# Optimization experiments

Hardware: AMD Instinct MI355X
Metric: run time of the kernel (lower is better)

Reference implementation:

```python
import jax, jax.numpy as jnp
import numpy as np
from jax import lax

D_MODEL=1024; D_STATE=128; D_CONV=4; EXPAND=2; HEADDIM=64
D_INNER=EXPAND*D_MODEL; NHEADS=D_INNER//HEADDIM
POOL=64; SUMDIM=256; TAU1=0.5; TAU2=0.4

def rmsnorm(x, w, eps):
    return x * lax.rsqrt(jnp.mean(x*x, axis=-1, keepdims=True) + eps) * w

def silu(x):
    return x * jax.nn.sigmoid(x)

def setup_inputs():
    key = jax.random.key(0)
    ks = jax.random.split(key, 20)
    B, T = 4, 2048
    d_in_proj = 2*D_INNER + 2*D_STATE + NHEADS
    inp = {
        'x': jax.random.normal(ks[0], (B, T, D_MODEL), jnp.float32),
        'pool': jnp.zeros((B, POOL, SUMDIM), jnp.float32),
        'priorities': jnp.zeros((B, POOL), jnp.float32),
        'counts': jnp.zeros((B,), jnp.int32),
        'norm_w': jnp.ones((D_MODEL,), jnp.float32),
        'in_w': jax.random.normal(ks[1], (d_in_proj, D_MODEL), jnp.float32)*0.02,
        'conv_w': jax.random.normal(ks[2], (D_INNER+2*D_STATE, 1, D_CONV), jnp.float32)*0.1,
        'conv_b': jnp.zeros((D_INNER+2*D_STATE,), jnp.float32),
        'dt_bias': jax.random.uniform(ks[3], (NHEADS,), jnp.float32, -5.0, -1.0),
        'A_log': jnp.log(jax.random.uniform(ks[4], (NHEADS,), jnp.float32, 1.0, 16.0)),
        'Dp': jax.random.normal(ks[5], (NHEADS,), jnp.float32)*0.1 + 1.0,
        'ssm_norm_w': jnp.ones((D_INNER,), jnp.float32),
        'out_w': jax.random.normal(ks[6], (D_MODEL, D_INNER), jnp.float32)*0.02,
        'score_w1': jax.random.normal(ks[7], (D_MODEL//4, D_MODEL), jnp.float32)*0.03,
        'score_w2': jax.random.normal(ks[8], (1, D_MODEL//4), jnp.float32)*0.06,
        'summ_w': jax.random.normal(ks[9], (SUMDIM, D_MODEL), jnp.float32)*0.03,
        'q_w': jax.random.normal(ks[10], (SUMDIM, D_MODEL), jnp.float32)*0.03,
        'k_w': jax.random.normal(ks[11], (SUMDIM, SUMDIM), jnp.float32)*0.06,
        'v_w': jax.random.normal(ks[12], (D_MODEL, SUMDIM), jnp.float32)*0.06,
        'gate_w': jax.random.normal(ks[13], (D_MODEL, 2*D_MODEL), jnp.float32)*0.02,
    }
    return inp

def mamba2(u, in_w, conv_w, conv_b, dt_bias, A_log, Dp, ssm_norm_w, out_w):
    B, T, _ = u.shape
    zxbcdt = u @ in_w.T                      # [B,T,2*d_inner+2*d_state+nheads]
    z = zxbcdt[..., :D_INNER]
    xBC = zxbcdt[..., D_INNER:2*D_INNER+2*D_STATE]
    dt = jax.nn.softplus(zxbcdt[..., 2*D_INNER+2*D_STATE:] + dt_bias)  # [B,T,H]
    # causal depthwise conv over time
    xc = jnp.transpose(xBC, (0, 2, 1))       # [B,C,T]
    xc = lax.conv_general_dilated(xc, conv_w, (1,), [(D_CONV-1, 0)],
                                  dimension_numbers=('NCH', 'OIH', 'NCH'),
                                  feature_group_count=D_INNER+2*D_STATE)
    xBC = silu(jnp.transpose(xc + conv_b[None, :, None], (0, 2, 1)))
    xh = xBC[..., :D_INNER].reshape(B, T, NHEADS, HEADDIM)
    Bm = xBC[..., D_INNER:D_INNER+D_STATE]   # [B,T,N]
    Cm = xBC[..., D_INNER+D_STATE:]          # [B,T,N]
    A = -jnp.exp(A_log)                      # [H]
    dA = jnp.exp(dt * A)                     # [B,T,H]
    def step(h, inp):
        dA_t, dt_t, x_t, B_t, C_t = inp      # [B,H],[B,H],[B,H,P],[B,N],[B,N]
        h = dA_t[:, :, None, None]*h + (dt_t[:, :, None]*x_t)[..., None]*B_t[:, None, None, :]
        y = jnp.einsum('bhpn,bn->bhp', h, C_t)
        return h, y
    h0 = jnp.zeros((B, NHEADS, HEADDIM, D_STATE), u.dtype)
    xs = (jnp.swapaxes(dA, 0, 1), jnp.swapaxes(dt, 0, 1), jnp.swapaxes(xh, 0, 1),
          jnp.swapaxes(Bm, 0, 1), jnp.swapaxes(Cm, 0, 1))
    _, ys = lax.scan(step, h0, xs)           # [T,B,H,P]
    y = jnp.swapaxes(ys, 0, 1) + Dp[None, None, :, None]*xh
    y = y.reshape(B, T, D_INNER)
    y = rmsnorm(y * silu(z), ssm_norm_w, 1e-5)
    return y @ out_w.T

def pool_update(tokens, scores, pool, priorities, counts,
                summ_w):
    B, T, D = tokens.shape
    mask = scores > TAU1
    order = jnp.argsort(-scores, axis=1)     # descending
    s_scores = jnp.take_along_axis(scores, order, 1)
    s_tokens = jnp.take_along_axis(tokens, order[..., None], 1)
    s_mask = jnp.take_along_axis(mask, order, 1)
    summaries = s_tokens @ summ_w.T          # [B,T,SUMDIM]
    nslots = min(T, POOL)
    bidx = jnp.arange(B)
    def slot_step(carry, inp):
        pool, pri, counts = carry
        has_imp, imp, summ = inp             # [B],[B],[B,SUMDIM]
        add = has_imp & (counts < POOL)
        widx = jnp.minimum(counts, POOL-1)
        pool = pool.at[bidx, widx].set(jnp.where(add[:, None], summ, pool[bidx, widx]))
        pri = pri.at[bidx, widx].set(jnp.where(add, imp, pri[bidx, widx]))
        counts = counts + add.astype(counts.dtype)
        replace = has_imp & (counts >= POOL)
        min_idx = jnp.argmin(pri, axis=1)
        min_p = pri[bidx, min_idx]
        should = replace & (imp > min_p)
        pool = pool.at[bidx, min_idx].set(jnp.where(should[:, None], summ, pool[bidx, min_idx]))
        pri = pri.at[bidx, min_idx].set(jnp.where(should, imp, pri[bidx, min_idx]))
        return (pool, pri, counts), None
    xs = (jnp.swapaxes(s_mask[:, :nslots], 0, 1),
          jnp.swapaxes(s_scores[:, :nslots], 0, 1),
          jnp.swapaxes(summaries[:, :nslots], 0, 1))
    (pool, priorities, counts), _ = lax.scan(slot_step, (pool, priorities, counts), xs)
    return pool, priorities, counts

def reference(x, pool, priorities, counts, norm_w, in_w, conv_w, conv_b, dt_bias,
              A_log, Dp, ssm_norm_w, out_w, score_w1, score_w2, summ_w,
              q_w, k_w, v_w, gate_w):
    B = x.shape[0]
    y = x + mamba2(rmsnorm(x, norm_w, 1e-4), in_w, conv_w, conv_b, dt_bias,
                   A_log, Dp, ssm_norm_w, out_w)
    scores = jax.nn.sigmoid(jnp.maximum(y @ score_w1.T, 0.0) @ score_w2.T)[..., 0]
    # layer_idx % cross_layer_frequency == 0 -> update path taken
    pool, priorities, counts = pool_update(y, scores, pool, priorities, counts, summ_w)
    mask = jnp.arange(POOL)[None, :] < counts[:, None]
    q = y @ q_w.T                            # [B,T,S]
    k = pool @ k_w.T                         # [B,P,S]
    v = pool @ v_w.T                         # [B,P,D]
    attn = jnp.einsum('bts,bps->btp', q, k) / (SUMDIM ** 0.5)
    attn = jnp.where(mask[:, None, :], attn, -jnp.inf)
    attn = jnp.nan_to_num(jax.nn.softmax(attn, axis=-1), nan=0.0)
    retrieved = jnp.einsum('btp,bpd->btd', attn, v)
    gate = jax.nn.sigmoid(jnp.concatenate([y, retrieved], axis=-1) @ gate_w.T)
    rmask = ((jnp.mean(scores, axis=1) > TAU2) & (counts > 0)).astype(y.dtype)[:, None, None]
    y = y + gate * retrieved * rmask
    return (y, pool, priorities, counts)
```

## Files before the change

kernel.cpp:

```cpp
#include <hip/hip_runtime.h>


using u16 = unsigned short;
using f16x8 = __attribute__((ext_vector_type(8))) _Float16;
using f32x4  = __attribute__((ext_vector_type(4))) float;

#define DEV __device__ __forceinline__

#define GLOAD4(g, l)  __builtin_amdgcn_global_load_lds((const __attribute__((address_space(1))) void*)(g), (__attribute__((address_space(3))) void*)(l), 4, 0, 0)
#define GLOAD16(g, l) __builtin_amdgcn_global_load_lds((const __attribute__((address_space(1))) void*)(g), (__attribute__((address_space(3))) void*)(l), 16, 0, 0)
#define VMWAIT(N) asm volatile("s_waitcnt vmcnt(" #N ")" ::: "memory")

static constexpr int Bb = 4, T = 2048, D = 1024;
static constexpr int DIN = 2048, DST = 128, NH = 32;
static constexpr int DPROJ = 4384;
static constexpr int CCH = 2304;
static constexpr int ROWS = Bb * T;
static constexpr int NC = 8, CL = 256;
static constexpr float RSC = 4096.f, RSCI = 1.f / 4096.f;

DEV u16 f2h_bits(float f) { union { _Float16 h; u16 u; } v; v.h = (_Float16)f; return v.u; }
DEV float h2f(u16 u) { union { _Float16 h; u16 u; } v; v.u = u; return (float)v.h; }
DEV double sigd(double x) { return 1.0 / (1.0 + exp(-x)); }
DEV float sigf(float x) { return 1.f / (1.f + expf(-x)); }
DEV int swz(int c) { return c ^ ((c >> 3) & 3); }

__global__ void diag_kernel(float* o, float v) { if (threadIdx.x == 0) o[0] = v; }
__global__ void zerod_kernel(double* p, int n) { if ((int)threadIdx.x < n) p[threadIdx.x] = 0.0; }

__global__ void split2_kernel(const float* __restrict__ in, u16* __restrict__ out, long n) {
    long i = (long)blockIdx.x * 256 + threadIdx.x;
    if (i >= n) return;
    float v = in[i];
    u16 h = f2h_bits(v);
    float r1 = (v - h2f(h)) * RSC;
    out[i] = h;
    out[n + i] = f2h_bits(r1);
}

__global__ __launch_bounds__(256) void rms_x_kernel(const float* __restrict__ x, const float* __restrict__ w,
                                                    u16* __restrict__ up, long pstride) {
    long row = blockIdx.x; int tid = threadIdx.x;
    const float* xr = x + row * D;
    float4 xv = *(const float4*)(xr + tid * 4);
    double ss = (double)xv.x * xv.x + (double)xv.y * xv.y + (double)xv.z * xv.z + (double)xv.w * xv.w;
    for (int off = 1; off < 64; off <<= 1) ss += __shfl_xor(ss, off);
    __shared__ double tmp[4];
    if ((tid & 63) == 0) tmp[tid >> 6] = ss;
    __syncthreads();
    double tot = tmp[0] + tmp[1] + tmp[2] + tmp[3];
    double scale = 1.0 / sqrt(tot / (double)D + 1e-4);
    float4 wv = *(const float4*)(w + tid * 4);
    long base = row * D + tid * 4;
    float vals[4];
    vals[0] = (float)((double)xv.x * scale * (double)wv.x);
    vals[1] = (float)((double)xv.y * scale * (double)wv.y);
    vals[2] = (float)((double)xv.z * scale * (double)wv.z);
    vals[3] = (float)((double)xv.w * scale * (double)wv.w);
#pragma unroll
    for (int j = 0; j < 4; j++) {
        float f = vals[j];
        u16 h = f2h_bits(f);
        up[base + j] = h;
        up[pstride + base + j] = f2h_bits((f - h2f(h)) * RSC);
    }
}

template <int NP>
DEV void stage_one(u16* s0, u16* s1, const float* __restrict__ src, long ld,
                   int row0, int lastrow, int k0, int tid) {
    int r = tid >> 1, cb = (tid & 1) * 2;
    long rg = row0 + r; if (rg > lastrow) rg = lastrow;
    const float* p = src + rg * ld + k0 + cb * 8;
    u16 h16[16], l16[16];
#pragma unroll
    for (int q = 0; q < 4; q++) {
        float4 v4 = *(const float4*)(p + q * 4);
        float vv[4] = { v4.x, v4.y, v4.z, v4.w };
#pragma unroll
        for (int j = 0; j < 4; j++) {
            float xv = vv[j];
            u16 h = f2h_bits(xv);
            h16[q * 4 + j] = h;
            if constexpr (NP == 2) l16[q * 4 + j] = f2h_bits((xv - h2f(h)) * RSC);
        }
    }
    int o0 = swz(r * 4 + cb) * 8, o1 = swz(r * 4 + cb + 1) * 8;
    *(uint4*)(s0 + o0) = *(const uint4*)(h16);
    *(uint4*)(s0 + o1) = *(const uint4*)(h16 + 8);
    if constexpr (NP == 2) {
        *(uint4*)(s1 + o0) = *(const uint4*)(l16);
        *(uint4*)(s1 + o1) = *(const uint4*)(l16 + 8);
    }
}

DEV void stage_pre_dma(u16* dst, const u16* __restrict__ src, long ld,
                       int row0, int lastrow, int k0, int wid, int lane) {
#pragma unroll
    for (int j = 0; j < 2; j++) {
        int s = wid * 128 + j * 64 + lane;
        int g = swz(s);
        int r = g >> 2, cs = g & 3;
        long rg = row0 + r; if (rg > lastrow) rg = lastrow;
        const u16* gp = src + rg * ld + k0 + cs * 8;
        GLOAD16(gp, dst + (wid * 128 + j * 64) * 8);
    }
}

#define STAGE_TILE(bb, k0_) do { \
    u16* As0_ = (bb); \
    u16* As1_ = (bb) + 4096; \
    u16* Bs0_ = (bb) + NP * 4096; \
    u16* Bs1_ = (bb) + NP * 4096 + 4096; \
    if constexpr (BP) { \
        stage_pre_dma(Bs0_, Bp, K, tN, N - 1, (k0_), wid, lane); \
        if constexpr (NP == 2) stage_pre_dma(Bs1_, Bp + bstride, K, tN, N - 1, (k0_), wid, lane); \
    } \
    if constexpr (AP) { \
        stage_pre_dma(As0_, Ap, K, tM, M - 1, (k0_), wid, lane); \
        if constexpr (NP == 2) stage_pre_dma(As1_, Ap + astride, K, tM, M - 1, (k0_), wid, lane); \
    } else { \
        stage_one<NP>(As0_, NP == 2 ? As1_ : nullptr, A, lda, tM, M - 1, (k0_), tid); \
    } \
    if constexpr (!BP) { \
        stage_one<NP>(Bs0_, NP == 2 ? Bs1_ : nullptr, B, ldb, tN, N - 1, (k0_), tid); \
    } \
} while (0)

template <int NP, int MODE, bool BP, bool AP>
__global__ __launch_bounds__(256, 2) void gemm_f32(
    const float* __restrict__ A, long lda,
    const u16* __restrict__ Ap, size_t astride,
    const float* __restrict__ B, long ldb,
    const u16* __restrict__ Bp, size_t bstride,
    int M, int N, int K,
    float* __restrict__ out0, float* __restrict__ out1,
    const float* __restrict__ aux0, const float* __restrict__ aux1,
    float* __restrict__ dtb, float* __restrict__ dab) {
    __shared__ __align__(16) u16 sm[2 * NP * 2 * 4096];
    int tid = threadIdx.x, lane = tid & 63, wid = tid >> 6;
    int wr = wid >> 1, wc = wid & 1;
    int nwg = gridDim.x * gridDim.y;
    int wg = blockIdx.y * gridDim.x + blockIdx.x;
    int lin = (wg & 7) * (nwg >> 3) + (wg >> 3);
    int tM = (lin / gridDim.x) * 128, tN = (lin % gridDim.x) * 128;

    f32x4 acc1[4][4], acc2[4][4];
#pragma unroll
    for (int i = 0; i < 4; i++)
#pragma unroll
        for (int j = 0; j < 4; j++) {
            acc1[i][j] = f32x4{0.f, 0.f, 0.f, 0.f};
            if constexpr (NP == 2) acc2[i][j] = f32x4{0.f, 0.f, 0.f, 0.f};
        }

    int rA = wr * 64 + (lane & 15);
    int rB = wc * 64 + (lane & 15);
    int kc = lane >> 4;
    int oA[4], oB[4];
#pragma unroll
    for (int i = 0; i < 4; i++) {
        oA[i] = swz((rA + i * 16) * 4 + kc) * 8;
        oB[i] = swz((rB + i * 16) * 4 + kc) * 8;
    }

    int nsteps = K / 32;
    int cur = 0;
    STAGE_TILE(sm, 0);
    __syncthreads();
    for (int kt = 0; kt < nsteps; ++kt) {
        u16* cb = sm + cur * (NP * 2 * 4096);
        if (kt + 1 < nsteps) {
            u16* nb = sm + (cur ^ 1) * (NP * 2 * 4096);
            STAGE_TILE(nb, (kt + 1) * 32);
        }
        u16* As0 = cb; u16* As1 = cb + 4096;
        u16* Bs0 = cb + NP * 4096; u16* Bs1 = cb + NP * 4096 + 4096;
        f16x8 fa[4], fb[4];
#pragma unroll
        for (int i = 0; i < 4; i++) {
            fa[i] = *(const f16x8*)(As0 + oA[i]);
            fb[i] = *(const f16x8*)(Bs0 + oB[i]);
        }
#pragma unroll
        for (int mi = 0; mi < 4; mi++)
#pragma unroll
            for (int ni = 0; ni < 4; ni++)
                acc1[mi][ni] = __builtin_amdgcn_mfma_f32_16x16x32_f16(fa[mi], fb[ni], acc1[mi][ni], 0, 0, 0);
        if constexpr (NP == 2) {
#pragma unroll
            for (int i = 0; i < 4; i++) fb[i] = *(const f16x8*)(Bs1 + oB[i]);
#pragma unroll
            for (int mi = 0; mi < 4; mi++)
#pragma unroll
                for (int ni = 0; ni < 4; ni++)
                    acc2[mi][ni] = __builtin_amdgcn_mfma_f32_16x16x32_f16(fa[mi], fb[ni], acc2[mi][ni], 0, 0, 0);
#pragma unroll
            for (int i = 0; i < 4; i++) {
                fa[i] = *(const f16x8*)(As1 + oA[i]);
                fb[i] = *(const f16x8*)(Bs0 + oB[i]);
            }
#pragma unroll
            for (int mi = 0; mi < 4; mi++)
#pragma unroll
                for (int ni = 0; ni < 4; ni++)
                    acc2[mi][ni] = __builtin_amdgcn_mfma_f32_16x16x32_f16(fa[mi], fb[ni], acc2[mi][ni], 0, 0, 0);
        }
        if (kt + 1 < nsteps) {
            __syncthreads();
            cur ^= 1;
        }
    }
    int laneh = lane >> 4, lanel = lane & 15;
#pragma unroll
    for (int mi = 0; mi < 4; mi++)
#pragma unroll
        for (int ni = 0; ni < 4; ni++) {
            int col = tN + wc * 64 + ni * 16 + lanel;
            if (col >= N) continue;
#pragma unroll
            for (int r = 0; r < 4; r++) {
                long row = tM + wr * 64 + mi * 16 + laneh * 4 + r;
                float v = acc1[mi][ni][r];
                if constexpr (NP == 2) v += acc2[mi][ni][r] * RSCI;
                if constexpr (MODE == 0) {
                    if (col < 2048) out0[row * 2048 + col] = v;
                    else if (col < 4352) out1[row * 2304 + (col - 2048)] = v;
                    else {
                        int h = col - 4352;
                        double xx = (double)v + (double)aux0[h];
                        double sp = (xx > 30.0) ? xx : log1p(exp(xx));
                        double a = -exp((double)aux1[h]);
                        dtb[row * NH + h] = (float)sp;
                        dab[row * NH + h] = (float)exp(sp * a);
                    }
                } else if constexpr (MODE == 1) {
                    out0[row * 256 + col] = fmaxf(v, 0.f);
                } else if constexpr (MODE == 2) {
                    float y = aux0[row * 1024 + col] + v;
                    out0[row * 1024 + col] = y;
                    out1[row * 2048 + col] = y;
                } else if constexpr (MODE == 3) {
                    out0[row * 256 + col] = v;
                } else {
                    double g = sigd((double)v);
                    float retr = aux0[row * 2048 + 1024 + col];
                    out0[row * 1024 + col] += (float)(g * (double)retr * (double)aux1[row >> 11]);
                }
            }
        }
}

__global__ __launch_bounds__(256) void conv_kernel(const float* __restrict__ xin, const float* __restrict__ cw,
                                                   const float* __restrict__ cb, float* __restrict__ xbc) {
    int blk = blockIdx.x;
    int ct = blk % 36; int tt = (blk / 36) % 32; int b = blk / (36 * 32);
    int c0 = ct * 64, t0 = tt * 64;
    int tid = threadIdx.x;
    __shared__ float tile[67 * 64];
    for (int i = tid; i < 67 * 64; i += 256) {
        int r = i >> 6, c = i & 63;
        int t = t0 - 3 + r;
        tile[i] = (t >= 0) ? xin[((long)(b * T + t)) * CCH + c0 + c] : 0.f;
    }
    __syncthreads();
    int c = tid & 63; int rb = (tid >> 6) * 16;
    int gc = c0 + c;
    float w0 = cw[gc * 4], w1 = cw[gc * 4 + 1], w2 = cw[gc * 4 + 2], w3 = cw[gc * 4 + 3];
    float bias = cb[gc];
    for (int j = 0; j < 16; j++) {
        int tl = rb + j;
        float a = bias + w0 * tile[tl * 64 + c] + w1 * tile[(tl + 1) * 64 + c]
                       + w2 * tile[(tl + 2) * 64 + c] + w3 * tile[(tl + 3) * 64 + c];
        xbc[((long)(b * T + t0 + tl)) * CCH + gc] = a * sigf(a);
    }
}

#define SCAN_STEP(tt) do { \
    int slot_ = (tt) & 7; \
    float dtv_ = sdt[(tt)], dav_ = sda[(tt)]; \
    float xt0_ = sx[slot_][pp], xt1_ = sx[slot_][pp + 8]; \
    float dtx0_ = dtv_ * xt0_, dtx1_ = dtv_ * xt1_; \
    const float4* BP_ = (const float4*)&sbc[slot_][0]; \
    float y0a_ = 0.f, y0b_ = 0.f, y1a_ = 0.f, y1b_ = 0.f; \
    _Pragma("unroll") \
    for (int r_ = 0; r_ < 4; r_++) { \
        float4 bv_ = BP_[r_ * 8 + sub]; \
        float4 cv_ = BP_[32 + r_ * 8 + sub]; \
        hs0[r_*4+0] = fmaf(dav_, hs0[r_*4+0], dtx0_ * bv_.x); y0a_ = fmaf(hs0[r_*4+0], cv_.x, y0a_); \
        hs0[r_*4+1] = fmaf(dav_, hs0[r_*4+1], dtx0_ * bv_.y); y0b_ = fmaf(hs0[r_*4+1], cv_.y, y0b_); \
        hs0[r_*4+2] = fmaf(dav_, hs0[r_*4+2], dtx0_ * bv_.z); y0a_ = fmaf(hs0[r_*4+2], cv_.z, y0a_); \
        hs0[r_*4+3] = fmaf(dav_, hs0[r_*4+3], dtx0_ * bv_.w); y0b_ = fmaf(hs0[r_*4+3], cv_.w, y0b_); \
        hs1[r_*4+0] = fmaf(dav_, hs1[r_*4+0], dtx1_ * bv_.x); y1a_ = fmaf(hs1[r_*4+0], cv_.x, y1a_); \
        hs1[r_*4+1] = fmaf(dav_, hs1[r_*4+1], dtx1_ * bv_.y); y1b_ = fmaf(hs1[r_*4+1], cv_.y, y1b_); \
        hs1[r_*4+2] = fmaf(dav_, hs1[r_*4+2], dtx1_ * bv_.z); y1a_ = fmaf(hs1[r_*4+2], cv_.z, y1a_); \
        hs1[r_*4+3] = fmaf(dav_, hs1[r_*4+3], dtx1_ * bv_.w); y1b_ = fmaf(hs1[r_*4+3], cv_.w, y1b_); \
    } \
    float y0_ = y0a_ + y0b_, y1_ = y1a_ + y1b_; \
    y0_ += __shfl_xor(y0_, 1); y0_ += __shfl_xor(y0_, 2); y0_ += __shfl_xor(y0_, 4); \
    y1_ += __shfl_xor(y1_, 1); y1_ += __shfl_xor(y1_, 2); y1_ += __shfl_xor(y1_, 4); \
    if (sub == 0) { \
        yout[(long)(tt) * DIN] = y0_ + sDp * xt0_; \
        yout[(long)(tt) * DIN + 8] = y1_ + sDp * xt1_; \
    } \
    runA *= dav_; \
    if (wrc && l == 0) cumAp[(tt)] = runA; \
} while (0)

#define SCAN_ISSUE(s) do { \
    GLOAD16(bcsrc + (long)(s) * CCH, &sbc[(s) & 7][0]); \
    GLOAD4(xsrc + (long)(s) * CCH, &sx[(s) & 7][0]); \
} while (0)

__global__ __launch_bounds__(64) void scan_kernel(const float* __restrict__ xbc, const float* __restrict__ dtb,
                                                  const float* __restrict__ dab, const float* __restrict__ Dp,
                                                  float* __restrict__ ys, float* __restrict__ hend,
                                                  float* __restrict__ cumA) {
    int bx = blockIdx.x;
    int b = bx >> 10, h = (bx >> 5) & 31, c = (bx >> 2) & 7, q4 = bx & 3;
    int l = threadIdx.x;
    int sub = l & 7, pp = l >> 3;
    __shared__ __align__(16) float sbc[8][256];
    __shared__ __align__(16) float sx[8][64];
    __shared__ float sdt[CL];
    __shared__ float sda[CL];
    long rowc = (long)b * T + (long)c * CL;
    const float* bcrow = xbc + rowc * CCH + 2048;
    const float* xrow  = xbc + rowc * CCH + h * 64 + q4 * 16;
    float* yout = ys + rowc * DIN + h * 64 + q4 * 16 + pp;

    int perm = ((l >> 3) & 3) | ((l & 7) << 2) | (l & 32);
    const float* bcsrc = bcrow + perm * 4;
    const float* xsrc  = xrow + (l & 15);

    bool wrc = (q4 == 0);
    float* cumAp = cumA + ((long)(b * 32 + h)) * T + (long)c * CL;
    float runA = 1.f;

    for (int i = 0; i < CL / 64; i++) {
        GLOAD4(dtb + (rowc + i * 64 + l) * NH + h, &sdt[i * 64]);
        GLOAD4(dab + (rowc + i * 64 + l) * NH + h, &sda[i * 64]);
    }
#pragma unroll
    for (int s = 0; s < 6; s++) SCAN_ISSUE(s);

    float hs0[16], hs1[16];
#pragma unroll
    for (int j = 0; j < 16; j++) { hs0[j] = 0.f; hs1[j] = 0.f; }
    float sDp = Dp[h];

    constexpr int NI = CL / 2;
    for (int i = 0; i < NI - 3; i++) {
        int s0 = 2 * i + 6;
        SCAN_ISSUE(s0);
        SCAN_ISSUE(s0 + 1);
        VMWAIT(12);
        SCAN_STEP(2 * i);
        SCAN_STEP(2 * i + 1);
    }
    { int i = NI - 3; VMWAIT(8); SCAN_STEP(2 * i); SCAN_STEP(2 * i + 1); }
    { int i = NI - 2; VMWAIT(4); SCAN_STEP(2 * i); SCAN_STEP(2 * i + 1); }
    { int i = NI - 1; VMWAIT(0); SCAN_STEP(2 * i); SCAN_STEP(2 * i + 1); }

    if (c < NC - 1) {
        float* hp = hend + (((long)(b * 32 + h)) * (NC - 1) + c) * 8192 + (q4 * 16 + pp) * 128 + sub * 16;
#pragma unroll
        for (int j = 0; j < 16; j += 4) *(float4*)(hp + j) = *(float4*)&hs0[j];
        float* hp1 = hp + 8 * 128;
#pragma unroll
        for (int j = 0; j < 16; j += 4) *(float4*)(hp1 + j) = *(float4*)&hs1[j];
    }
}

__global__ __launch_bounds__(256) void scanfix_kernel(float* __restrict__ hend, const float* __restrict__ cumA) {
    int bh = blockIdx.x; int tid = threadIdx.x;
    float P[NC - 1];
#pragma unroll
    for (int c = 1; c < NC - 1; c++) P[c] = cumA[(long)bh * T + (long)(c + 1) * CL - 1];
    float* hb = hend + (long)bh * (NC - 1) * 8192;
    for (int e = tid; e < 8192; e += 256) {
        float acc = hb[e];
#pragma unroll
        for (int c = 1; c < NC - 1; c++) {
            acc = fmaf(P[c], acc, hb[(long)c * 8192 + e]);
            hb[(long)c * 8192 + e] = acc;
        }
    }
}

__global__ __launch_bounds__(256) void scancorr_kernel(const float* __restrict__ hend, const float* __restrict__ cumA,
                                                       const float* __restrict__ xbc, float* __restrict__ ys) {
    int blk = blockIdx.x;
    constexpr int TQ = CL / 128;
    int tq = blk % TQ;
    int cm = (blk / TQ) % (NC - 1);
    int bh = blk / (TQ * (NC - 1));
    int b = bh >> 5, h = bh & 31;
    int tid = threadIdx.x;
    int p = tid >> 2, nq = tid & 3;
    const float* Hin = hend + ((long)bh * (NC - 1) + cm) * 8192 + p * 128 + nq * 32;
    float hreg[32];
#pragma unroll
    for (int j = 0; j < 32; j += 4) *(float4*)&hreg[j] = *(const float4*)(Hin + j);
    __shared__ float sC[8][128];
    long t0 = (long)(cm + 1) * CL + tq * 128;
    const float* cA = cumA + (long)bh * T;
    for (int tg = 0; tg < 16; tg++) {
        __syncthreads();
        {
            int tt = tg * 8 + (tid >> 5);
            int cc = (tid & 31) * 4;
            *(float4*)&sC[tid >> 5][cc] = *(const float4*)(xbc + ((long)b * T + t0 + tt) * CCH + 2176 + cc);
        }
        __syncthreads();
#pragma unroll
        for (int j = 0; j < 8; j++) {
            long t = t0 + tg * 8 + j;
            const float* Cr = &sC[j][nq * 32];
            float d = 0.f;
#pragma unroll
            for (int k = 0; k < 32; k += 4) {
                float4 cv = *(const float4*)(Cr + k);
                d += hreg[k] * cv.x + hreg[k + 1] * cv.y + hreg[k + 2] * cv.z + hreg[k + 3] * cv.w;
            }
            d += __shfl_xor(d, 1);
            d += __shfl_xor(d, 2);
            if (nq == 0) {
                float ca = cA[t];
                ys[((long)b * T + t) * DIN + h * 64 + p] += ca * d;
            }
        }
    }
}

__global__ __launch_bounds__(256) void ssmnorm_kernel(float* __restrict__ ys, const float* __restrict__ z,
                                                      const float* __restrict__ w) {
    long row = blockIdx.x; int tid = threadIdx.x;
    float* yr = ys + row * DIN;
    const float* zr = z + row * DIN;
    float v[8]; float ss = 0.f;
#pragma unroll
    for (int j = 0; j < 8; j++) {
        int c = tid * 8 + j;
        float zz = zr[c];
        float val = yr[c] * (zz * sigf(zz));
        v[j] = val; ss = fmaf(val, val, ss);
    }
    for (int off = 1; off < 64; off <<= 1) ss += __shfl_xor(ss, off);
    __shared__ float tmp[4];
    if ((tid & 63) == 0) tmp[tid >> 6] = ss;
    __syncthreads();
    float tot = tmp[0] + tmp[1] + tmp[2] + tmp[3];
    float scale = 1.f / sqrtf(tot * (1.f / (float)DIN) + 1e-5f);
#pragma unroll
    for (int j = 0; j < 8; j++) {
        int c = tid * 8 + j;
        yr[c] = v[j] * scale * w[c];
    }
}

__global__ void score2_kernel(const float* __restrict__ sh, const float* __restrict__ w2,
                              float* __restrict__ scores, double* __restrict__ ssum) {
    int row = blockIdx.x * 4 + (threadIdx.x >> 6);
    int lane = threadIdx.x & 63;
    const float* h = sh + (long)row * 256;
    double a = 0.0;
    for (int j = 0; j < 4; j++) a += (double)h[lane * 4 + j] * (double)w2[lane * 4 + j];
    for (int off = 1; off < 64; off <<= 1) a += __shfl_xor(a, off);
    if (lane == 0) {
        double sc = sigd(a);
        scores[row] = (float)sc;
        atomicAdd(&ssum[row >> 11], sc);
    }
}

__global__ __launch_bounds__(256) void top64_kernel(const float* __restrict__ scores, int* __restrict__ tidx,
                                                    float* __restrict__ tval) {
    int b = blockIdx.x; int tid = threadIdx.x;
    int lane = tid & 63, wid = tid >> 6;
    float v[8];
#pragma unroll
    for (int j = 0; j < 8; j++) v[j] = scores[b * T + tid + j * 256];
    __shared__ float wv[4];
    __shared__ int wi[4];
    __shared__ int sbesti;
    for (int k = 0; k < 64; k++) {
        float lv = -1e30f; int li = 1 << 30;
#pragma unroll
        for (int j = 0; j < 8; j++) {
            int ii = tid + j * 256;
            if (v[j] > lv) { lv = v[j]; li = ii; }
        }
        for (int off = 1; off < 64; off <<= 1) {
            float ov = __shfl_xor(lv, off); int oi = __shfl_xor(li, off);
            if (ov > lv || (ov == lv && oi < li)) { lv = ov; li = oi; }
        }
        if (lane == 0) { wv[wid] = lv; wi[wid] = li; }
        __syncthreads();
        if (tid == 0) {
            float bv = wv[0]; int bi = wi[0];
#pragma unroll
            for (int w = 1; w < 4; w++)
                if (wv[w] > bv || (wv[w] == bv && wi[w] < bi)) { bv = wv[w]; bi = wi[w]; }
            tidx[b * 64 + k] = bi;
            tval[b * 64 + k] = bv;
            sbesti = bi;
        }
        __syncthreads();
        int bi = sbesti;
        if ((bi & 255) == tid) {
            int jj = bi >> 8;
#pragma unroll
            for (int j = 0; j < 8; j++) if (j == jj) v[j] = -1e30f;
        }
    }
}

__global__ __launch_bounds__(256) void summ_kernel(const float* __restrict__ y, const int* __restrict__ tidx,
                                                   const float* __restrict__ wsum, float* __restrict__ summ) {
    int s = blockIdx.x & 63; int b = blockIdx.x >> 6;
    int tid = threadIdx.x;
    __shared__ float yrow[1024];
    int tok = tidx[b * 64 + s];
    long base = ((long)(b * T + tok));
    for (int i = tid; i < 1024; i += 256) yrow[i] = y[base * 1024 + i];
    __syncthreads();
    double acc = 0.0;
    const float* w = wsum + (long)tid * 1024;
    for (int kk = 0; kk < 1024; kk++) acc += (double)yrow[kk] * (double)w[kk];
    summ[((long)(b * 64 + s)) * 256 + tid] = (float)acc;
}

__global__ void pool_kernel(const float* __restrict__ pin, const float* __restrict__ prin,
                            const int* __restrict__ cin, const float* __restrict__ tval,
                            const float* __restrict__ summ, const double* __restrict__ ssum,
                            float* __restrict__ pout, float* __restrict__ prout,
                            float* __restrict__ cout, float* __restrict__ rmask) {
    int b = blockIdx.x; int tid = threadIdx.x;
    __shared__ float spri[64];
    __shared__ int scount, sact, sslot, srep, srslot;
    for (int i = tid; i < 64 * 256; i += 256) pout[(long)b * 16384 + i] = pin[(long)b * 16384 + i];
    if (tid < 64) spri[tid] = prin[b * 64 + tid];
    if (tid == 0) scount = cin[b];
    __syncthreads();
    for (int s = 0; s < 64; s++) {
        float imp = tval[b * 64 + s];
        bool has = imp > 0.5f;
        if (tid == 0) {
            sact = 0;
            if (has && scount < 64) { sslot = scount; spri[scount] = imp; scount++; sact = 1; }
        }
        __syncthreads();
        if (sact) pout[((long)(b * 64 + sslot)) * 256 + tid] = summ[((long)(b * 64 + s)) * 256 + tid];
        if (tid < 64) {
            float v = spri[tid]; int idx = tid;
            for (int off = 1; off < 64; off <<= 1) {
                float v2 = __shfl_xor(v, off); int i2 = __shfl_xor(idx, off);
                if (v2 < v || (v2 == v && i2 < idx)) { v = v2; idx = i2; }
            }
            if (tid == 0) {
                srep = 0;
                if (has && scount >= 64 && imp > v) { srep = 1; srslot = idx; spri[idx] = imp; }
            }
        }
        __syncthreads();
        if (srep) pout[((long)(b * 64 + srslot)) * 256 + tid] = summ[((long)(b * 64 + s)) * 256 + tid];
    }
    __syncthreads();
    if (tid < 64) prout[b * 64 + tid] = spri[tid];
    if (tid == 0) {
        cout[b] = (float)scount;
        double mean = ssum[b] / (double)T;
        rmask[b] = (mean > 0.4 && scount > 0) ? 1.f : 0.f;
    }
}

__global__ __launch_bounds__(256) void kv_kernel(const float* __restrict__ pool, const float* __restrict__ kw,
                                                 const float* __restrict__ vw, float* __restrict__ k,
                                                 float* __restrict__ v) {
    int blk = blockIdx.x; int b = blk >> 6, s = blk & 63; int tid = threadIdx.x;
    __shared__ float pr[256];
    pr[tid] = pool[((long)(b * 64 + s)) * 256 + tid];
    __syncthreads();
    float a = 0.f;
    const float* w = kw + (long)tid * 256;
    for (int j = 0; j < 256; j++) a = fmaf(pr[j], w[j], a);
    k[((long)(b * 64 + s)) * 256 + tid] = a;
    for (int m = 0; m < 4; m++) {
        int o = m * 256 + tid;
        const float* w2 = vw + (long)o * 256;
        float c = 0.f;
        for (int j = 0; j < 256; j++) c = fmaf(pr[j], w2[j], c);
        v[((long)(b * 64 + s)) * 1024 + o] = c;
    }
}

__global__ __launch_bounds__(256) void attn_kernel(const float* __restrict__ q, const float* __restrict__ k,
                                                   const float* __restrict__ v, const float* __restrict__ cout,
                                                   float* __restrict__ concat) {
    long row = blockIdx.x;
    int b = (int)(row >> 11);
    int tid = threadIdx.x;
    int cnt = (int)cout[b];
    __shared__ float qs[256], slog[64], sp[64];
    qs[tid] = q[row * 256 + tid];
    __syncthreads();
    int s = tid >> 2, part = tid & 3;
    const float* kr = k + ((long)(b * 64 + s)) * 256 + part * 64;
    float d = 0.f;
    for (int j = 0; j < 64; j++) d = fmaf(qs[part * 64 + j], kr[j], d);
    d += __shfl_xor(d, 1); d += __shfl_xor(d, 2);
    if (part == 0) slog[s] = d * 0.0625f;
    __syncthreads();
    if (tid < 64) {
        float l = (tid < cnt) ? slog[tid] : -1e30f;
        float m = l;
        for (int off = 1; off < 64; off <<= 1) m = fmaxf(m, __shfl_xor(m, off));
        float e = (tid < cnt) ? expf(l - m) : 0.f;
        float su = e;
        for (int off = 1; off < 64; off <<= 1) su += __shfl_xor(su, off);
        sp[tid] = (cnt > 0) ? e / su : 0.f;
    }
    __syncthreads();
    float acc[4] = {0.f, 0.f, 0.f, 0.f};
    for (int s2 = 0; s2 < cnt; s2++) {
        float p = sp[s2];
        const float* vr = v + ((long)(b * 64 + s2)) * 1024 + tid;
        acc[0] = fmaf(p, vr[0], acc[0]);
        acc[1] = fmaf(p, vr[256], acc[1]);
        acc[2] = fmaf(p, vr[512], acc[2]);
        acc[3] = fmaf(p, vr[768], acc[3]);
    }
    for (int j = 0; j < 4; j++) concat[row * 2048 + 1024 + tid + j * 256] = acc[j];
}

extern "C" void kernel_launch(void* const* d_in, const int* in_sizes, int n_in,
                              void* d_out, int out_size, void* d_ws, size_t ws_size,
                              hipStream_t stream) {
    (void)in_sizes; (void)n_in; (void)out_size;
    const float* x       = (const float*)d_in[0];
    const float* pool_in = (const float*)d_in[1];
    const float* pri_in  = (const float*)d_in[2];
    const int*   cnt_in  = (const int*)d_in[3];
    const float* norm_w  = (const float*)d_in[4];
    const float* in_w    = (const float*)d_in[5];
    const float* conv_w  = (const float*)d_in[6];
    const float* conv_b  = (const float*)d_in[7];
    const float* dt_bias = (const float*)d_in[8];
    const float* A_log   = (const float*)d_in[9];
    const float* Dp      = (const float*)d_in[10];
    const float* ssm_w   = (const float*)d_in[11];
    const float* out_w   = (const float*)d_in[12];
    const float* s_w1    = (const float*)d_in[13];
    const float* s_w2    = (const float*)d_in[14];
    const float* summ_w  = (const float*)d_in[15];
    const float* q_w     = (const float*)d_in[16];
    const float* k_w     = (const float*)d_in[17];
    const float* v_w     = (const float*)d_in[18];
    const float* gate_w  = (const float*)d_in[19];

    float* outy    = (float*)d_out;
    float* outpool = outy + (long)ROWS * D;
    float* outpri  = outpool + Bb * 64 * 256;
    float* outcnt  = outpri + Bb * 64;

    char* ws = (char*)d_ws;
    size_t cur = 0;
    auto alloc = [&](size_t bytes) { size_t o = cur; cur += (bytes + 255) / 256 * 256; return o; };

    size_t pw_in_bytes   = (size_t)2 * DPROJ * 1024 * 2;
    size_t ra_bytes = (size_t)ROWS * CCH * 4;

    size_t o_dt   = alloc((size_t)ROWS * NH * 4);
    size_t o_da   = alloc((size_t)ROWS * NH * 4);
    size_t o_sc   = alloc((size_t)ROWS * 4);
    size_t o_ssum = alloc(64);
    size_t o_rmk  = alloc(64);
    size_t o_tidx = alloc(Bb * 64 * 4);
    size_t o_tval = alloc(Bb * 64 * 4);
    size_t o_summ = alloc((size_t)Bb * 64 * 256 * 4);
    size_t o_k    = alloc((size_t)Bb * 64 * 256 * 4);
    size_t o_v    = alloc((size_t)Bb * 64 * 1024 * 4);
    size_t o_cumA = alloc((size_t)128 * T * 4);
    size_t o_RA = alloc(ra_bytes);
    size_t o_RB = alloc((size_t)ROWS * DIN * 4);
    size_t o_RC = alloc((size_t)ROWS * CCH * 4);

    if (ws_size < cur) {
        diag_kernel<<<1, 64, 0, stream>>>(outy, 1000.0f + (float)(ws_size >> 20));
        return;
    }

    float* dtb    = (float*)(ws + o_dt);
    float* dab    = (float*)(ws + o_da);
    float* scores = (float*)(ws + o_sc);
    double* ssum  = (double*)(ws + o_ssum);
    float* rmk    = (float*)(ws + o_rmk);
    int*   tidx   = (int*)(ws + o_tidx);
    float* tval   = (float*)(ws + o_tval);
    float* summ   = (float*)(ws + o_summ);
    float* kbuf   = (float*)(ws + o_k);
    float* vbuf   = (float*)(ws + o_v);
    float* cumA   = (float*)(ws + o_cumA);
    float* hend   = outy;

    u16*  pw_in   = (u16*)(ws + o_RA);
    u16*  uplanes = (u16*)(ws + o_RA + pw_in_bytes);
    float* xbc    = (float*)(ws + o_RA);
    float* concat = (float*)(ws + o_RA);
    float* sch    = (float*)(ws + o_RA + (size_t)ROWS * DIN * 4);
    float* bufZ   = (float*)(ws + o_RB);
    u16*  pw_out  = (u16*)(ws + o_RB);
    u16*  pw_s1   = (u16*)(ws + o_RB + (size_t)16 * 1024 * 1024);
    float* qbuf   = (float*)(ws + o_RB);
    float* bufX   = (float*)(ws + o_RC);
    float* yscan  = (float*)(ws + o_RC);

    zerod_kernel<<<1, 64, 0, stream>>>(ssum, 4);
    {
        long n = (long)DPROJ * 1024;
        split2_kernel<<<(n + 255) / 256, 256, 0, stream>>>(in_w, pw_in, n);
    }
    rms_x_kernel<<<ROWS, 256, 0, stream>>>(x, norm_w, uplanes, (long)ROWS * D);
    gemm_f32<2, 0, true, true><<<dim3(35, 64), 256, 0, stream>>>(
        nullptr, 0, uplanes, (size_t)ROWS * D,
        nullptr, 0, pw_in, (size_t)DPROJ * 1024,
        ROWS, DPROJ, 1024,
        bufZ, bufX, dt_bias, A_log, dtb, dab);
    conv_kernel<<<Bb * 32 * 36, 256, 0, stream>>>(bufX, conv_w, conv_b, xbc);
    scan_kernel<<<Bb * NH * NC * 4, 64, 0, stream>>>(xbc, dtb, dab, Dp, yscan, hend, cumA);
    scanfix_kernel<<<128, 256, 0, stream>>>(hend, cumA);
    scancorr_kernel<<<128 * (NC - 1) * (CL / 128), 256, 0, stream>>>(hend, cumA, xbc, yscan);
    ssmnorm_kernel<<<ROWS, 256, 0, stream>>>(yscan, bufZ, ssm_w);
    {
        long n = (long)1024 * 2048;
        split2_kernel<<<(n + 255) / 256, 256, 0, stream>>>(out_w, pw_out, n);
        long n2 = (long)256 * 1024;
        split2_kernel<<<(n2 + 255) / 256, 256, 0, stream>>>(s_w1, pw_s1, n2);
    }
    gemm_f32<2, 2, true, false><<<dim3(8, 64), 256, 0, stream>>>(
        yscan, 2048, nullptr, 0,
        nullptr, 0, pw_out, (size_t)1024 * 2048,
        ROWS, 1024, 2048,
        outy, concat, x, nullptr, nullptr, nullptr);
    gemm_f32<2, 1, true, false><<<dim3(2, 64), 256, 0, stream>>>(
        outy, 1024, nullptr, 0,
        nullptr, 0, pw_s1, (size_t)256 * 1024,
        ROWS, 256, 1024,
        sch, nullptr, nullptr, nullptr, nullptr, nullptr);
    score2_kernel<<<ROWS / 4, 256, 0, stream>>>(sch, s_w2, scores, ssum);
    top64_kernel<<<Bb, 256, 0, stream>>>(scores, tidx, tval);
    summ_kernel<<<Bb * 64, 256, 0, stream>>>(outy, tidx, summ_w, summ);
    pool_kernel<<<Bb, 256, 0, stream>>>(pool_in, pri_in, cnt_in, tval, summ, ssum,
                                        outpool, outpri, outcnt, rmk);
    kv_kernel<<<Bb * 64, 256, 0, stream>>>(outpool, k_w, v_w, kbuf, vbuf);
    gemm_f32<1, 3, false, false><<<dim3(2, 64), 256, 0, stream>>>(
        outy, 1024, nullptr, 0,
        q_w, 1024, nullptr, 0,
        ROWS, 256, 1024,
        qbuf, nullptr, nullptr, nullptr, nullptr, nullptr);
    attn_kernel<<<ROWS, 256, 0, stream>>>(qbuf, kbuf, vbuf, outcnt, concat);
    gemm_f32<1, 4, false, false><<<dim3(8, 64), 256, 0, stream>>>(
        concat, 2048, nullptr, 0,
        gate_w, 2048, nullptr, 0,
        ROWS, 1024, 2048,
        outy, nullptr, concat, rmk, nullptr, nullptr);
}
```

Before: 1.646 ms.

## Vectorize elementwise kernel loads and merge small launches

Folds the ssum zeroing kernel into the first split2 launch and merges the two weight-split launches into one dual kernel. The conv tile load, ssmnorm, score2 and summ kernels switch to float4 vector loads and stores. The goal is fewer kernel launches and fewer memory transactions in small memory-bound kernels. The order of double-precision accumulation is unchanged.

Measured after the change: 1.628 ms. About the same (-1.1%).

```diff
diff --git a/kernel.cpp b/kernel.cpp
--- a/kernel.cpp
+++ b/kernel.cpp
@@ -26,16 +26,34 @@
 DEV int swz(int c) { return c ^ ((c >> 3) & 3); }
 
 __global__ void diag_kernel(float* o, float v) { if (threadIdx.x == 0) o[0] = v; }
-__global__ void zerod_kernel(double* p, int n) { if ((int)threadIdx.x < n) p[threadIdx.x] = 0.0; }
-
-__global__ void split2_kernel(const float* __restrict__ in, u16* __restrict__ out, long n) {
+
+__global__ void split2_kernel(const float* __restrict__ in, u16* __restrict__ out, long n,
+                              double* __restrict__ ssum) {
     long i = (long)blockIdx.x * 256 + threadIdx.x;
+    if (ssum && blockIdx.x == 0 && threadIdx.x < 4) ssum[threadIdx.x] = 0.0;
     if (i >= n) return;
     float v = in[i];
     u16 h = f2h_bits(v);
     float r1 = (v - h2f(h)) * RSC;
     out[i] = h;
     out[n + i] = f2h_bits(r1);
+}
+
+__global__ void split2_dual_kernel(const float* __restrict__ a, u16* __restrict__ oa, long na,
+                                   const float* __restrict__ b2, u16* __restrict__ ob, long nb) {
+    long i = (long)blockIdx.x * 256 + threadIdx.x;
+    if (i < na) {
+        float v = a[i];
+        u16 h = f2h_bits(v);
+        oa[i] = h;
+        oa[na + i] = f2h_bits((v - h2f(h)) * RSC);
+    } else if (i < na + nb) {
+        long j = i - na;
+        float v = b2[j];
+        u16 h = f2h_bits(v);
+        ob[j] = h;
+        ob[nb + j] = f2h_bits((v - h2f(h)) * RSC);
+    }
 }
 
 __global__ __launch_bounds__(256) void rms_x_kernel(const float* __restrict__ x, const float* __restrict__ w,
@@ -258,10 +276,12 @@
     int c0 = ct * 64, t0 = tt * 64;
     int tid = threadIdx.x;
     __shared__ float tile[67 * 64];
-    for (int i = tid; i < 67 * 64; i += 256) {
-        int r = i >> 6, c = i & 63;
+    for (int i = tid; i < 67 * 16; i += 256) {
+        int r = i >> 4, c4 = i & 15;
         int t = t0 - 3 + r;
-        tile[i] = (t >= 0) ? xin[((long)(b * T + t)) * CCH + c0 + c] : 0.f;
+        float4 v = (t >= 0) ? *(const float4*)(xin + ((long)(b * T + t)) * CCH + c0 + c4 * 4)
+                            : float4{0.f, 0.f, 0.f, 0.f};
+        *(float4*)&tile[r * 64 + c4 * 4] = v;
     }
     __syncthreads();
     int c = tid & 63; int rb = (tid >> 6) * 16;
@@ -438,12 +458,17 @@
     long row = blockIdx.x; int tid = threadIdx.x;
     float* yr = ys + row * DIN;
     const float* zr = z + row * DIN;
+    float4 yv0 = *(const float4*)(yr + tid * 8);
+    float4 yv1 = *(const float4*)(yr + tid * 8 + 4);
+    float4 zv0 = *(const float4*)(zr + tid * 8);
+    float4 zv1 = *(const float4*)(zr + tid * 8 + 4);
+    float yv[8] = { yv0.x, yv0.y, yv0.z, yv0.w, yv1.x, yv1.y, yv1.z, yv1.w };
+    float zv[8] = { zv0.x, zv0.y, zv0.z, zv0.w, zv1.x, zv1.y, zv1.z, zv1.w };
     float v[8]; float ss = 0.f;
 #pragma unroll
     for (int j = 0; j < 8; j++) {
-        int c = tid * 8 + j;
-        float zz = zr[c];
-        float val = yr[c] * (zz * sigf(zz));
+        float zz = zv[j];
+        float val = yv[j] * (zz * sigf(zz));
         v[j] = val; ss = fmaf(val, val, ss);
     }
     for (int off = 1; off < 64; off <<= 1) ss += __shfl_xor(ss, off);
@@ -452,20 +477,26 @@
     __syncthreads();
     float tot = tmp[0] + tmp[1] + tmp[2] + tmp[3];
     float scale = 1.f / sqrtf(tot * (1.f / (float)DIN) + 1e-5f);
-#pragma unroll
-    for (int j = 0; j < 8; j++) {
-        int c = tid * 8 + j;
-        yr[c] = v[j] * scale * w[c];
-    }
+    float4 wv0 = *(const float4*)(w + tid * 8);
+    float4 wv1 = *(const float4*)(w + tid * 8 + 4);
+    float wv[8] = { wv0.x, wv0.y, wv0.z, wv0.w, wv1.x, wv1.y, wv1.z, wv1.w };
+    float o[8];
+#pragma unroll
+    for (int j = 0; j < 8; j++) o[j] = v[j] * scale * wv[j];
+    *(float4*)(yr + tid * 8)     = float4{ o[0], o[1], o[2], o[3] };
+    *(float4*)(yr + tid * 8 + 4) = float4{ o[4], o[5], o[6], o[7] };
 }
 
 __global__ void score2_kernel(const float* __restrict__ sh, const float* __restrict__ w2,
                               float* __restrict__ scores, double* __restrict__ ssum) {
     int row = blockIdx.x * 4 + (threadIdx.x >> 6);
     int lane = threadIdx.x & 63;
-    const float* h = sh + (long)row * 256;
-    double a = 0.0;
-    for (int j = 0; j < 4; j++) a += (double)h[lane * 4 + j] * (double)w2[lane * 4 + j];
+    float4 hv = *(const float4*)(sh + (long)row * 256 + lane * 4);
+    float4 wv = *(const float4*)(w2 + lane * 4);
+    double a = (double)hv.x * (double)wv.x;
+    a += (double)hv.y * (double)wv.y;
+    a += (double)hv.z * (double)wv.z;
+    a += (double)hv.w * (double)wv.w;
     for (int off = 1; off < 64; off <<= 1) a += __shfl_xor(a, off);
     if (lane == 0) {
         double sc = sigd(a);
@@ -523,11 +554,20 @@
     __shared__ float yrow[1024];
     int tok = tidx[b * 64 + s];
     long base = ((long)(b * T + tok));
-    for (int i = tid; i < 1024; i += 256) yrow[i] = y[base * 1024 + i];
+    {
+        float4 vv = *(const float4*)(y + base * 1024 + tid * 4);
+        *(float4*)&yrow[tid * 4] = vv;
+    }
     __syncthreads();
     double acc = 0.0;
     const float* w = wsum + (long)tid * 1024;
-    for (int kk = 0; kk < 1024; kk++) acc += (double)yrow[kk] * (double)w[kk];
+    for (int kk = 0; kk < 1024; kk += 4) {
+        float4 wv = *(const float4*)(w + kk);
+        acc += (double)yrow[kk] * (double)wv.x;
+        acc += (double)yrow[kk + 1] * (double)wv.y;
+        acc += (double)yrow[kk + 2] * (double)wv.z;
+        acc += (double)yrow[kk + 3] * (double)wv.w;
+    }
     summ[((long)(b * 64 + s)) * 256 + tid] = (float)acc;
 }
 
@@ -716,10 +756,9 @@
     float* bufX   = (float*)(ws + o_RC);
     float* yscan  = (float*)(ws + o_RC);
 
-    zerod_kernel<<<1, 64, 0, stream>>>(ssum, 4);
     {
         long n = (long)DPROJ * 1024;
-        split2_kernel<<<(n + 255) / 256, 256, 0, stream>>>(in_w, pw_in, n);
+        split2_kernel<<<(n + 255) / 256, 256, 0, stream>>>(in_w, pw_in, n, ssum);
     }
     rms_x_kernel<<<ROWS, 256, 0, stream>>>(x, norm_w, uplanes, (long)ROWS * D);
     gemm_f32<2, 0, true, true><<<dim3(35, 64), 256, 0, stream>>>(
@@ -734,9 +773,9 @@
     ssmnorm_kernel<<<ROWS, 256, 0, stream>>>(yscan, bufZ, ssm_w);
     {
         long n = (long)1024 * 2048;
-        split2_kernel<<<(n + 255) / 256, 256, 0, stream>>>(out_w, pw_out, n);
         long n2 = (long)256 * 1024;
-        split2_kernel<<<(n2 + 255) / 256, 256, 0, stream>>>(s_w1, pw_s1, n2);
+        split2_dual_kernel<<<(int)((n + n2 + 255) / 256), 256, 0, stream>>>(
+            out_w, pw_out, n, s_w1, pw_s1, n2);
     }
     gemm_f32<2, 2, true, false><<<dim3(8, 64), 256, 0, stream>>>(
         yscan, 2048, nullptr, 0,
```
